# Optimization experiments

Measured on AMD Instinct MI355X. Metric: run time of the kernel, lower is better.

The kernel has to match this reference:

```python
import jax, jax.numpy as jnp
import numpy as np

N = 100000      # nodes
E = 3200000     # directed edges (avg degree 32)
F_IN, HID, CLS = 512, 256, 64


def setup_inputs() -> dict:
    key = jax.random.key(0)
    k = jax.random.split(key, 6)
    x = jax.random.normal(k[0], (N, F_IN), dtype=jnp.float32)
    edge_index = jax.random.randint(k[1], (2, E), 0, N, dtype=jnp.int32)
    W1 = jax.random.normal(k[2], (F_IN, HID), dtype=jnp.float32) / np.float32(np.sqrt(F_IN))
    b1 = jnp.zeros((HID,), dtype=jnp.float32)
    W2 = jax.random.normal(k[3], (HID, CLS), dtype=jnp.float32) / np.float32(np.sqrt(HID))
    b2 = jnp.zeros((CLS,), dtype=jnp.float32)
    return {"x": x, "edge_index": edge_index, "W1": W1, "b1": b1, "W2": W2, "b2": b2}


def gcn_layer(x, W, b, src, dst, n):
    """GCN layer: out = D^{-1/2} (A + I) D^{-1/2} (x W + b)."""
    h = x @ W + b                                   # [n, out]
    loop = jnp.arange(n, dtype=src.dtype)
    s = jnp.concatenate([src, loop])                # add self loops
    d = jnp.concatenate([dst, loop])
    deg = jax.ops.segment_sum(jnp.ones_like(d, dtype=h.dtype), d, num_segments=n)
    dinv = jax.lax.rsqrt(jnp.maximum(deg, 1.0))
    norm = dinv[s] * dinv[d]                        # [E+n]
    return jax.ops.segment_sum(h[s] * norm[:, None], d, num_segments=n)


def reference(x, edge_index, W1, b1, W2, b2):
    src, dst = edge_index[0], edge_index[1]
    n = x.shape[0]
    h = jax.nn.relu(gcn_layer(x, W1, b1, src, dst, n))
    # dropout is identity in eval mode
    h = gcn_layer(h, W2, b2, src, dst, n)
    return jax.nn.log_softmax(h, axis=1)
```

## Files before the change

kernel.cpp:

```cpp
#include <hip/hip_runtime.h>

#define FIN 512
#define HID 256
#define CLS 64
#define PAD 8
#define BKT_SLACK 4096

typedef short bf16x8 __attribute__((ext_vector_type(8)));
typedef float f32x4 __attribute__((ext_vector_type(4)));
typedef float f32x2 __attribute__((ext_vector_type(2)));

__device__ __forceinline__ float bf2f(unsigned short u) {
    union { unsigned int i; float f; } c; c.i = ((unsigned int)u) << 16; return c.f;
}
__device__ __forceinline__ unsigned short f2bf(float f) {
    union { float f; unsigned int u; } c; c.f = f;
    unsigned int u = c.u;
    return (unsigned short)((u + 0x7fffu + ((u >> 16) & 1u)) >> 16);
}
__device__ __forceinline__ unsigned char f2fp8(float v) {
    int r = __builtin_amdgcn_cvt_pk_fp8_f32(v, v, 0, false);
    return (unsigned char)(r & 0xFF);
}


__global__ __launch_bounds__(256) void k_hist(const int* __restrict__ dst,
                                              int* __restrict__ bktcnt, int E) {
    __shared__ int h[256];
    h[threadIdx.x] = 0;
    __syncthreads();
    for (int i = blockIdx.x * blockDim.x + threadIdx.x; i < E; i += gridDim.x * blockDim.x)
        atomicAdd(&h[dst[i] >> 9], 1);
    __syncthreads();
    if (h[threadIdx.x]) atomicAdd(&bktcnt[threadIdx.x], h[threadIdx.x]);
}

__global__ __launch_bounds__(256) void k_bktscan(const int* __restrict__ bktcnt,
                                                 int* __restrict__ bkt_base,
                                                 int* __restrict__ bkt_cursor,
                                                 int NB, int E) {
    __shared__ int sh[256];
    int t = threadIdx.x;
    int v = (t < NB) ? bktcnt[t] : 0;
    sh[t] = v;
    __syncthreads();
    for (int s = 1; s < 256; s <<= 1) {
        int u = (t >= s) ? sh[t - s] : 0;
        __syncthreads();
        sh[t] += u;
        __syncthreads();
    }
    int excl = sh[t] - v;
    if (t < NB) { bkt_base[t] = excl; bkt_cursor[t] = excl; }
    if (t == 0) bkt_base[NB] = E;
}

#define EPB 4096
__global__ __launch_bounds__(256) void k_binscatter(
        const int* __restrict__ src, const int* __restrict__ dst,
        int* __restrict__ bkt_cursor, uint2* __restrict__ ebuf, int E) {
    __shared__ int h[256];
    __shared__ int cb[256];
    int t = threadIdx.x;
    h[t] = 0;
    __syncthreads();
    int base = blockIdx.x * EPB;
    int es[16], ed[16], lp[16];
    #pragma unroll
    for (int it = 0; it < 16; ++it) {
        int i = base + it * 256 + t;
        if (i < E) {
            es[it] = src[i];
            ed[it] = dst[i];
            lp[it] = atomicAdd(&h[ed[it] >> 9], 1);
        } else {
            es[it] = -1; ed[it] = 0; lp[it] = 0;
        }
    }
    __syncthreads();
    int c = h[t];
    if (c) cb[t] = atomicAdd(&bkt_cursor[t], c);
    __syncthreads();
    #pragma unroll
    for (int it = 0; it < 16; ++it) {
        if (es[it] >= 0) {
            int b = ed[it] >> 9;
            ebuf[cb[b] + lp[it]] = make_uint2((unsigned)es[it], (unsigned)ed[it]);
        }
    }
}

__global__ __launch_bounds__(256) void k_csrbuild(
        const uint2* __restrict__ ebuf, const int* __restrict__ bkt_base,
        int* __restrict__ rs, int* __restrict__ cnte, float* __restrict__ dinv,
        int* __restrict__ csr, int Nn) {
    __shared__ int deg[512];
    __shared__ int cur[512];
    __shared__ int ts[256];
    int b = blockIdx.x, t = threadIdx.x;
    int e0 = bkt_base[b], e1 = bkt_base[b + 1];
    int pb = e0 + b * BKT_SLACK;
    int node0 = b << 9;
    deg[t] = 0; deg[t + 256] = 0;
    __syncthreads();
    for (int j = e0 + t; j < e1; j += 256)
        atomicAdd(&deg[(int)ebuf[j].y - node0], 1);
    __syncthreads();
    int n0 = node0 + 2 * t;
    int d0 = deg[2 * t], d1 = deg[2 * t + 1];
    int p0 = (n0 < Nn)     ? ((d0 + 1 + PAD - 1) & ~(PAD - 1)) : 0;
    int p1 = (n0 + 1 < Nn) ? ((d1 + 1 + PAD - 1) & ~(PAD - 1)) : 0;
    ts[t] = p0 + p1;
    __syncthreads();
    for (int s = 1; s < 256; s <<= 1) {
        int u = (t >= s) ? ts[t - s] : 0;
        __syncthreads();
        ts[t] += u;
        __syncthreads();
    }
    int excl = ts[t] - (p0 + p1);
    cur[2 * t] = excl;
    cur[2 * t + 1] = excl + p0;
    if (n0 < Nn)     { rs[n0]     = pb + excl;      cnte[n0]     = p0; dinv[n0]     = rsqrtf((float)(d0 + 1)); }
    if (n0 + 1 < Nn) { rs[n0 + 1] = pb + excl + p0; cnte[n0 + 1] = p1; dinv[n0 + 1] = rsqrtf((float)(d1 + 1)); }
    __syncthreads();
    for (int j = e0 + t; j < e1; j += 256) {
        uint2 e = ebuf[j];
        int p = atomicAdd(&cur[(int)e.y - node0], 1);
        csr[pb + p] = (int)e.x;
    }
    if (n0 < Nn) {
        csr[pb + excl + d0] = n0;
        for (int j = d0 + 1; j < p0; ++j) csr[pb + excl + j] = Nn;
    }
    if (n0 + 1 < Nn) {
        csr[pb + excl + p0 + d1] = n0 + 1;
        for (int j = d1 + 1; j < p1; ++j) csr[pb + excl + p0 + j] = Nn;
    }
}

__global__ void k_wpack(const float* __restrict__ W, unsigned short* __restrict__ Wp,
                        int K, int Ncols) {
    int i = blockIdx.x * blockDim.x + threadIdx.x;
    if (i < K * Ncols) {
        int k = i / Ncols, n = i - k * Ncols;
        Wp[((size_t)(k >> 3) * Ncols + n) * 8 + (k & 7)] = f2bf(W[i]);
    }
}

__global__ __launch_bounds__(512) void k_gemm1(
        const float* __restrict__ x, const unsigned short* __restrict__ W1p,
        const float* __restrict__ b1, const float* __restrict__ dinv,
        unsigned char* __restrict__ hs1, int Nn) {
    __shared__ unsigned short As[64][40];
    int tid = threadIdx.x;
    int w = tid >> 6, lane = tid & 63;
    int wr = w >> 2, wc = w & 3;
    int l15 = lane & 15, l4 = lane >> 4;
    int row0 = blockIdx.x * 64;

    f32x4 zero = {0.f, 0.f, 0.f, 0.f};
    f32x4 acc[2][4];
    #pragma unroll
    for (int m = 0; m < 2; ++m)
        #pragma unroll
        for (int n = 0; n < 4; ++n) acc[m][n] = zero;

    int sr = tid >> 3;
    int sc = tid & 7;
    bool srok = (row0 + sr) < Nn;
    const float* xrow = x + (size_t)(row0 + sr) * FIN + sc * 4;

    for (int kt = 0; kt < FIN; kt += 32) {
        float4 v = srok ? *(const float4*)(xrow + kt) : make_float4(0.f, 0.f, 0.f, 0.f);
        ushort4 o;
        o.x = f2bf(v.x); o.y = f2bf(v.y); o.z = f2bf(v.z); o.w = f2bf(v.w);
        *(ushort4*)&As[sr][sc * 4] = o;
        __syncthreads();

        bf16x8 bfr[4];
        size_t bbase = (size_t)((kt >> 3) + l4) * HID * 8;
        #pragma unroll
        for (int n = 0; n < 4; ++n) {
            int col = wc * 64 + n * 16 + l15;
            bfr[n] = *(const bf16x8*)&W1p[bbase + (size_t)col * 8];
        }
        bf16x8 afr[2];
        #pragma unroll
        for (int m = 0; m < 2; ++m) {
            int r = wr * 32 + m * 16 + l15;
            afr[m] = *(const bf16x8*)&As[r][l4 * 8];
        }
        #pragma unroll
        for (int m = 0; m < 2; ++m)
            #pragma unroll
            for (int n = 0; n < 4; ++n)
                acc[m][n] = __builtin_amdgcn_mfma_f32_16x16x32_bf16(
                    afr[m], bfr[n], acc[m][n], 0, 0, 0);
        __syncthreads();
    }

    float b1c[4];
    #pragma unroll
    for (int n = 0; n < 4; ++n) b1c[n] = b1[wc * 64 + n * 16 + l15];
    #pragma unroll
    for (int m = 0; m < 2; ++m) {
        #pragma unroll
        for (int r = 0; r < 4; ++r) {
            int row = row0 + wr * 32 + m * 16 + l4 * 4 + r;
            if (row < Nn) {
                float dv = dinv[row];
                #pragma unroll
                for (int n = 0; n < 4; ++n) {
                    int col = wc * 64 + n * 16 + l15;
                    hs1[(size_t)row * HID + col] = f2fp8((acc[m][n][r] + b1c[n]) * dv);
                }
            }
        }
    }
}

__global__ __launch_bounds__(256) void k_agg1(
        const unsigned char* __restrict__ hs1, const int* __restrict__ csr,
        const int* __restrict__ rs, const int* __restrict__ cnte,
        const float* __restrict__ dinv, unsigned short* __restrict__ h2in, int Nn) {
    int d = blockIdx.x * 4 + (threadIdx.x >> 6);
    if (d >= Nn) return;
    int lane = threadIdx.x & 63;
    int g = lane >> 4, c = lane & 15;
    size_t coff = (size_t)c * 16;
    float acc[16];
    #pragma unroll
    for (int j = 0; j < 16; ++j) acc[j] = 0.f;
    int base = rs[d], cnt = cnte[d];
    const int* cp = csr + base;
    int t = 0;
    for (; t + 16 <= cnt; t += 16) {
        int i0 = cp[t + g], i1 = cp[t + 4 + g], i2 = cp[t + 8 + g], i3 = cp[t + 12 + g];
        uint4 v0 = *(const uint4*)&hs1[(size_t)i0 * HID + coff];
        uint4 v1 = *(const uint4*)&hs1[(size_t)i1 * HID + coff];
        uint4 v2 = *(const uint4*)&hs1[(size_t)i2 * HID + coff];
        uint4 v3 = *(const uint4*)&hs1[(size_t)i3 * HID + coff];
        unsigned int w0[4] = {v0.x, v0.y, v0.z, v0.w};
        unsigned int w1[4] = {v1.x, v1.y, v1.z, v1.w};
        unsigned int w2[4] = {v2.x, v2.y, v2.z, v2.w};
        unsigned int w3[4] = {v3.x, v3.y, v3.z, v3.w};
        #pragma unroll
        for (int k = 0; k < 4; ++k) {
            f32x2 a0 = __builtin_amdgcn_cvt_pk_f32_fp8(w0[k], false);
            f32x2 b0 = __builtin_amdgcn_cvt_pk_f32_fp8(w0[k], true);
            f32x2 a1 = __builtin_amdgcn_cvt_pk_f32_fp8(w1[k], false);
            f32x2 b1v = __builtin_amdgcn_cvt_pk_f32_fp8(w1[k], true);
            f32x2 a2 = __builtin_amdgcn_cvt_pk_f32_fp8(w2[k], false);
            f32x2 b2v = __builtin_amdgcn_cvt_pk_f32_fp8(w2[k], true);
            f32x2 a3 = __builtin_amdgcn_cvt_pk_f32_fp8(w3[k], false);
            f32x2 b3 = __builtin_amdgcn_cvt_pk_f32_fp8(w3[k], true);
            acc[k*4+0] += (a0[0] + a1[0]) + (a2[0] + a3[0]);
            acc[k*4+1] += (a0[1] + a1[1]) + (a2[1] + a3[1]);
            acc[k*4+2] += (b0[0] + b1v[0]) + (b2v[0] + b3[0]);
            acc[k*4+3] += (b0[1] + b1v[1]) + (b2v[1] + b3[1]);
        }
    }
    if (t < cnt) {
        int i0 = cp[t + g], i1 = cp[t + 4 + g];
        uint4 v0 = *(const uint4*)&hs1[(size_t)i0 * HID + coff];
        uint4 v1 = *(const uint4*)&hs1[(size_t)i1 * HID + coff];
        unsigned int w0[4] = {v0.x, v0.y, v0.z, v0.w};
        unsigned int w1[4] = {v1.x, v1.y, v1.z, v1.w};
        #pragma unroll
        for (int k = 0; k < 4; ++k) {
            f32x2 a0 = __builtin_amdgcn_cvt_pk_f32_fp8(w0[k], false);
            f32x2 b0 = __builtin_amdgcn_cvt_pk_f32_fp8(w0[k], true);
            f32x2 a1 = __builtin_amdgcn_cvt_pk_f32_fp8(w1[k], false);
            f32x2 b1v = __builtin_amdgcn_cvt_pk_f32_fp8(w1[k], true);
            acc[k*4+0] += a0[0] + a1[0];
            acc[k*4+1] += a0[1] + a1[1];
            acc[k*4+2] += b0[0] + b1v[0];
            acc[k*4+3] += b0[1] + b1v[1];
        }
    }
    #pragma unroll
    for (int j = 0; j < 16; ++j) {
        acc[j] += __shfl_xor(acc[j], 16);
        acc[j] += __shfl_xor(acc[j], 32);
    }
    float dv = dinv[d];
    ushort4 o;
    o.x = f2bf(fmaxf(acc[g * 4 + 0] * dv, 0.f));
    o.y = f2bf(fmaxf(acc[g * 4 + 1] * dv, 0.f));
    o.z = f2bf(fmaxf(acc[g * 4 + 2] * dv, 0.f));
    o.w = f2bf(fmaxf(acc[g * 4 + 3] * dv, 0.f));
    *(ushort4*)&h2in[(size_t)d * HID + c * 16 + g * 4] = o;
}

__global__ __launch_bounds__(256) void k_gemm2(
        const unsigned short* __restrict__ h2in, const unsigned short* __restrict__ W2p,
        const float* __restrict__ b2, const float* __restrict__ dinv,
        unsigned short* __restrict__ hs2, int Nn) {
    int tid = threadIdx.x;
    int w = tid >> 6, lane = tid & 63;
    int l15 = lane & 15, l4 = lane >> 4;
    int r0 = blockIdx.x * 64 + w * 16;
    int arow = r0 + l15;
    bool aok = arow < Nn;
    const unsigned short* ap = h2in + (size_t)arow * HID + l4 * 8;

    f32x4 zero = {0.f, 0.f, 0.f, 0.f};
    bf16x8 zf = {0, 0, 0, 0, 0, 0, 0, 0};
    f32x4 acc[4];
    #pragma unroll
    for (int n = 0; n < 4; ++n) acc[n] = zero;

    #pragma unroll
    for (int kt = 0; kt < HID; kt += 32) {
        bf16x8 a = aok ? *(const bf16x8*)(ap + kt) : zf;
        size_t bbase = (size_t)((kt >> 3) + l4) * CLS * 8;
        #pragma unroll
        for (int n = 0; n < 4; ++n) {
            bf16x8 bb = *(const bf16x8*)&W2p[bbase + (size_t)(n * 16 + l15) * 8];
            acc[n] = __builtin_amdgcn_mfma_f32_16x16x32_bf16(a, bb, acc[n], 0, 0, 0);
        }
    }
    float b2c[4];
    #pragma unroll
    for (int n = 0; n < 4; ++n) b2c[n] = b2[n * 16 + l15];
    #pragma unroll
    for (int r = 0; r < 4; ++r) {
        int row = r0 + l4 * 4 + r;
        if (row < Nn) {
            float dv = dinv[row];
            #pragma unroll
            for (int n = 0; n < 4; ++n)
                hs2[(size_t)row * CLS + n * 16 + l15] = f2bf((acc[n][r] + b2c[n]) * dv);
        }
    }
}

__global__ __launch_bounds__(256) void k_agg2(
        const unsigned short* __restrict__ hs2, const int* __restrict__ csr,
        const int* __restrict__ rs, const int* __restrict__ cnte,
        const float* __restrict__ dinv, float* __restrict__ out, int Nn) {
    int d = blockIdx.x * 4 + (threadIdx.x >> 6);
    if (d >= Nn) return;
    int lane = threadIdx.x & 63;
    int q = lane >> 4, c4 = lane & 15;
    size_t loff = (size_t)c4 * 4;
    float a0 = 0.f, a1 = 0.f, a2 = 0.f, a3 = 0.f;
    int base = rs[d], cnt = cnte[d];
    const int* cp = csr + base;
    int t = 0;
    for (; t + 16 <= cnt; t += 16) {
        int s0 = cp[t + q], s1 = cp[t + q + 4], s2 = cp[t + q + 8], s3 = cp[t + q + 12];
        ushort4 v0 = *(const ushort4*)&hs2[(size_t)s0 * CLS + loff];
        ushort4 v1 = *(const ushort4*)&hs2[(size_t)s1 * CLS + loff];
        ushort4 v2 = *(const ushort4*)&hs2[(size_t)s2 * CLS + loff];
        ushort4 v3 = *(const ushort4*)&hs2[(size_t)s3 * CLS + loff];
        a0 += (bf2f(v0.x) + bf2f(v1.x)) + (bf2f(v2.x) + bf2f(v3.x));
        a1 += (bf2f(v0.y) + bf2f(v1.y)) + (bf2f(v2.y) + bf2f(v3.y));
        a2 += (bf2f(v0.z) + bf2f(v1.z)) + (bf2f(v2.z) + bf2f(v3.z));
        a3 += (bf2f(v0.w) + bf2f(v1.w)) + (bf2f(v2.w) + bf2f(v3.w));
    }
    if (t < cnt) {
        int s0 = cp[t + q], s1 = cp[t + q + 4];
        ushort4 v0 = *(const ushort4*)&hs2[(size_t)s0 * CLS + loff];
        ushort4 v1 = *(const ushort4*)&hs2[(size_t)s1 * CLS + loff];
        a0 += bf2f(v0.x) + bf2f(v1.x);
        a1 += bf2f(v0.y) + bf2f(v1.y);
        a2 += bf2f(v0.z) + bf2f(v1.z);
        a3 += bf2f(v0.w) + bf2f(v1.w);
    }
    a0 += __shfl_xor(a0, 16); a0 += __shfl_xor(a0, 32);
    a1 += __shfl_xor(a1, 16); a1 += __shfl_xor(a1, 32);
    a2 += __shfl_xor(a2, 16); a2 += __shfl_xor(a2, 32);
    a3 += __shfl_xor(a3, 16); a3 += __shfl_xor(a3, 32);
    float dv = dinv[d];
    float y0 = a0 * dv, y1 = a1 * dv, y2 = a2 * dv, y3 = a3 * dv;
    float m = fmaxf(fmaxf(y0, y1), fmaxf(y2, y3));
    #pragma unroll
    for (int o = 1; o <= 8; o <<= 1) m = fmaxf(m, __shfl_xor(m, o));
    float s = __expf(y0 - m) + __expf(y1 - m) + __expf(y2 - m) + __expf(y3 - m);
    #pragma unroll
    for (int o = 1; o <= 8; o <<= 1) s += __shfl_xor(s, o);
    if (q == 0) {
        float lg = __logf(s);
        float4 o4 = make_float4(y0 - m - lg, y1 - m - lg, y2 - m - lg, y3 - m - lg);
        *(float4*)&out[(size_t)d * CLS + c4 * 4] = o4;
    }
}

extern "C" void kernel_launch(void* const* d_in, const int* in_sizes, int n_in,
                              void* d_out, int out_size, void* d_ws, size_t ws_size,
                              hipStream_t stream) {
    const float* x  = (const float*)d_in[0];
    const int* ei   = (const int*)d_in[1];
    const float* W1 = (const float*)d_in[2];
    const float* b1 = (const float*)d_in[3];
    const float* W2 = (const float*)d_in[4];
    const float* b2 = (const float*)d_in[5];
    float* out = (float*)d_out;

    const int N = in_sizes[0] / FIN;
    const int E = in_sizes[1] / 2;
    const int NB = (N + 511) >> 9;
    const int* srcp = ei;
    const int* dstp = ei + E;

    char* w = (char*)d_ws;
    auto alloc = [&](size_t bytes) -> void* {
        void* p = (void*)w;
        w += (bytes + 255) / 256 * 256;
        return p;
    };
    int* rs        = (int*)alloc((size_t)(N + 1) * 4);
    int* cnte      = (int*)alloc((size_t)N * 4);
    float* dinv    = (float*)alloc((size_t)N * 4);
    int* csr       = (int*)alloc(((size_t)E + (size_t)N + (size_t)NB * BKT_SLACK + 8) * 4);
    int* bktcnt    = (int*)alloc((size_t)(NB + 1) * 4);
    int* bkt_base  = (int*)alloc((size_t)(NB + 1) * 4);
    int* bkt_cursor= (int*)alloc((size_t)(NB + 1) * 4);
    size_t hs1_bytes = (size_t)N * HID + HID;
    size_t ebuf_bytes = (size_t)E * 8;
    unsigned char* hs1 = (unsigned char*)alloc(hs1_bytes > ebuf_bytes ? hs1_bytes : ebuf_bytes + HID);
    unsigned short* h2in = (unsigned short*)alloc((size_t)N * HID * 2);
    unsigned short* hs2  = (unsigned short*)alloc((size_t)(N + 1) * CLS * 2);
    unsigned short* W1p  = (unsigned short*)alloc((size_t)FIN * HID * 2);
    unsigned short* W2p  = (unsigned short*)alloc((size_t)HID * CLS * 2);
    uint2* ebuf = (uint2*)hs1;

    hipMemsetAsync(bktcnt, 0, (size_t)(NB + 1) * 4, stream);

    k_hist<<<1024, 256, 0, stream>>>(dstp, bktcnt, E);
    k_bktscan<<<1, 256, 0, stream>>>(bktcnt, bkt_base, bkt_cursor, NB, E);
    k_binscatter<<<(E + EPB - 1) / EPB, 256, 0, stream>>>(srcp, dstp, bkt_cursor, ebuf, E);
    k_csrbuild<<<NB, 256, 0, stream>>>(ebuf, bkt_base, rs, cnte, dinv, csr, N);

    hipMemsetAsync(hs1 + (size_t)N * HID, 0, HID, stream);
    hipMemsetAsync(hs2 + (size_t)N * CLS, 0, CLS * 2, stream);

    k_wpack<<<(FIN * HID + 255) / 256, 256, 0, stream>>>(W1, W1p, FIN, HID);
    k_wpack<<<(HID * CLS + 255) / 256, 256, 0, stream>>>(W2, W2p, HID, CLS);

    k_gemm1<<<(N + 63) / 64, 512, 0, stream>>>(x, W1p, b1, dinv, hs1, N);
    k_agg1<<<(N + 3) / 4, 256, 0, stream>>>(hs1, csr, rs, cnte, dinv, h2in, N);
    k_gemm2<<<(N + 63) / 64, 256, 0, stream>>>(h2in, W2p, b2, dinv, hs2, N);
    k_agg2<<<(N + 3) / 4, 256, 0, stream>>>(hs2, csr, rs, cnte, dinv, out, N);
}
```

Baseline: 404.3 us.

## Split layer-1 features into column chunks for cache-resident aggregation passes

```diff
diff --git a/kernel.cpp b/kernel.cpp
--- a/kernel.cpp
+++ b/kernel.cpp
@@ -5,10 +5,12 @@
 #define CLS 64
 #define PAD 8
 #define BKT_SLACK 4096
+#define NCHUNK 8
 
 typedef short bf16x8 __attribute__((ext_vector_type(8)));
 typedef float f32x4 __attribute__((ext_vector_type(4)));
 typedef float f32x2 __attribute__((ext_vector_type(2)));
+typedef unsigned int u32x2 __attribute__((ext_vector_type(2)));
 
 __device__ __forceinline__ float bf2f(unsigned short u) {
     union { unsigned int i; float f; } c; c.i = ((unsigned int)u) << 16; return c.f;
@@ -58,7 +60,7 @@
 #define EPB 4096
 __global__ __launch_bounds__(256) void k_binscatter(
         const int* __restrict__ src, const int* __restrict__ dst,
-        int* __restrict__ bkt_cursor, uint2* __restrict__ ebuf, int E) {
+        int* __restrict__ bkt_cursor, unsigned* __restrict__ ebuf, int E) {
     __shared__ int h[256];
     __shared__ int cb[256];
     int t = threadIdx.x;
@@ -85,13 +87,13 @@
     for (int it = 0; it < 16; ++it) {
         if (es[it] >= 0) {
             int b = ed[it] >> 9;
-            ebuf[cb[b] + lp[it]] = make_uint2((unsigned)es[it], (unsigned)ed[it]);
+            ebuf[cb[b] + lp[it]] = (unsigned)es[it] | ((unsigned)(ed[it] & 511) << 23);
         }
     }
 }
 
 __global__ __launch_bounds__(256) void k_csrbuild(
-        const uint2* __restrict__ ebuf, const int* __restrict__ bkt_base,
+        const unsigned* __restrict__ ebuf, const int* __restrict__ bkt_base,
         int* __restrict__ rs, int* __restrict__ cnte, float* __restrict__ dinv,
         int* __restrict__ csr, int Nn) {
     __shared__ int deg[512];
@@ -104,7 +106,7 @@
     deg[t] = 0; deg[t + 256] = 0;
     __syncthreads();
     for (int j = e0 + t; j < e1; j += 256)
-        atomicAdd(&deg[(int)ebuf[j].y - node0], 1);
+        atomicAdd(&deg[ebuf[j] >> 23], 1);
     __syncthreads();
     int n0 = node0 + 2 * t;
     int d0 = deg[2 * t], d1 = deg[2 * t + 1];
@@ -125,9 +127,9 @@
     if (n0 + 1 < Nn) { rs[n0 + 1] = pb + excl + p0; cnte[n0 + 1] = p1; dinv[n0 + 1] = rsqrtf((float)(d1 + 1)); }
     __syncthreads();
     for (int j = e0 + t; j < e1; j += 256) {
-        uint2 e = ebuf[j];
-        int p = atomicAdd(&cur[(int)e.y - node0], 1);
-        csr[pb + p] = (int)e.x;
+        unsigned e = ebuf[j];
+        int p = atomicAdd(&cur[e >> 23], 1);
+        csr[pb + p] = (int)(e & 0x7FFFFFu);
     }
     if (n0 < Nn) {
         csr[pb + excl + d0] = n0;
@@ -158,6 +160,7 @@
     int wr = w >> 2, wc = w & 3;
     int l15 = lane & 15, l4 = lane >> 4;
     int row0 = blockIdx.x * 64;
+    size_t cstride = (size_t)(Nn + 1) * 32;
 
     f32x4 zero = {0.f, 0.f, 0.f, 0.f};
     f32x4 acc[2][4];
@@ -208,89 +211,69 @@
         #pragma unroll
         for (int r = 0; r < 4; ++r) {
             int row = row0 + wr * 32 + m * 16 + l4 * 4 + r;
-            if (row < Nn) {
-                float dv = dinv[row];
-                #pragma unroll
-                for (int n = 0; n < 4; ++n) {
-                    int col = wc * 64 + n * 16 + l15;
-                    hs1[(size_t)row * HID + col] = f2fp8((acc[m][n][r] + b1c[n]) * dv);
-                }
+            if (row > Nn) continue;
+            float dv = (row < Nn) ? dinv[row] : 0.f;
+            #pragma unroll
+            for (int n = 0; n < 4; ++n) {
+                int col = wc * 64 + n * 16 + l15;
+                unsigned char val = (row < Nn)
+                    ? f2fp8((acc[m][n][r] + b1c[n]) * dv) : (unsigned char)0;
+                hs1[(size_t)(col >> 5) * cstride + (size_t)row * 32 + (col & 31)] = val;
             }
         }
     }
 }
 
-__global__ __launch_bounds__(256) void k_agg1(
-        const unsigned char* __restrict__ hs1, const int* __restrict__ csr,
-        const int* __restrict__ rs, const int* __restrict__ cnte,
-        const float* __restrict__ dinv, unsigned short* __restrict__ h2in, int Nn) {
+__global__ __launch_bounds__(256) void k_agg1c(
+        const unsigned char* __restrict__ hs1c,
+        const int* __restrict__ csr, const int* __restrict__ rs,
+        const int* __restrict__ cnte, const float* __restrict__ dinv,
+        unsigned short* __restrict__ h2in, int Nn, int chunk) {
     int d = blockIdx.x * 4 + (threadIdx.x >> 6);
     if (d >= Nn) return;
     int lane = threadIdx.x & 63;
-    int g = lane >> 4, c = lane & 15;
-    size_t coff = (size_t)c * 16;
-    float acc[16];
-    #pragma unroll
-    for (int j = 0; j < 16; ++j) acc[j] = 0.f;
+    int g = lane >> 3;
+    int f = lane & 7;
     int base = rs[d], cnt = cnte[d];
     const int* cp = csr + base;
+    float a0 = 0.f, a1 = 0.f, a2 = 0.f, a3 = 0.f;
     int t = 0;
     for (; t + 16 <= cnt; t += 16) {
-        int i0 = cp[t + g], i1 = cp[t + 4 + g], i2 = cp[t + 8 + g], i3 = cp[t + 12 + g];
-        uint4 v0 = *(const uint4*)&hs1[(size_t)i0 * HID + coff];
-        uint4 v1 = *(const uint4*)&hs1[(size_t)i1 * HID + coff];
-        uint4 v2 = *(const uint4*)&hs1[(size_t)i2 * HID + coff];
-        uint4 v3 = *(const uint4*)&hs1[(size_t)i3 * HID + coff];
-        unsigned int w0[4] = {v0.x, v0.y, v0.z, v0.w};
-        unsigned int w1[4] = {v1.x, v1.y, v1.z, v1.w};
-        unsigned int w2[4] = {v2.x, v2.y, v2.z, v2.w};
-        unsigned int w3[4] = {v3.x, v3.y, v3.z, v3.w};
-        #pragma unroll
-        for (int k = 0; k < 4; ++k) {
-            f32x2 a0 = __builtin_amdgcn_cvt_pk_f32_fp8(w0[k], false);
-            f32x2 b0 = __builtin_amdgcn_cvt_pk_f32_fp8(w0[k], true);
-            f32x2 a1 = __builtin_amdgcn_cvt_pk_f32_fp8(w1[k], false);
-            f32x2 b1v = __builtin_amdgcn_cvt_pk_f32_fp8(w1[k], true);
-            f32x2 a2 = __builtin_amdgcn_cvt_pk_f32_fp8(w2[k], false);
-            f32x2 b2v = __builtin_amdgcn_cvt_pk_f32_fp8(w2[k], true);
-            f32x2 a3 = __builtin_amdgcn_cvt_pk_f32_fp8(w3[k], false);
-            f32x2 b3 = __builtin_amdgcn_cvt_pk_f32_fp8(w3[k], true);
-            acc[k*4+0] += (a0[0] + a1[0]) + (a2[0] + a3[0]);
-            acc[k*4+1] += (a0[1] + a1[1]) + (a2[1] + a3[1]);
-            acc[k*4+2] += (b0[0] + b1v[0]) + (b2v[0] + b3[0]);
-            acc[k*4+3] += (b0[1] + b1v[1]) + (b2v[1] + b3[1]);
-        }
+        int i0 = __builtin_nontemporal_load(&cp[t + g]);
+        int i1 = __builtin_nontemporal_load(&cp[t + 8 + g]);
+        unsigned v0 = *(const unsigned*)&hs1c[(size_t)i0 * 32 + f * 4];
+        unsigned v1 = *(const unsigned*)&hs1c[(size_t)i1 * 32 + f * 4];
+        f32x2 p00 = __builtin_amdgcn_cvt_pk_f32_fp8(v0, false);
+        f32x2 p01 = __builtin_amdgcn_cvt_pk_f32_fp8(v0, true);
+        f32x2 p10 = __builtin_amdgcn_cvt_pk_f32_fp8(v1, false);
+        f32x2 p11 = __builtin_amdgcn_cvt_pk_f32_fp8(v1, true);
+        a0 += p00[0] + p10[0];
+        a1 += p00[1] + p10[1];
+        a2 += p01[0] + p11[0];
+        a3 += p01[1] + p11[1];
     }
     if (t < cnt) {
-        int i0 = cp[t + g], i1 = cp[t + 4 + g];
-        uint4 v0 = *(const uint4*)&hs1[(size_t)i0 * HID + coff];
-        uint4 v1 = *(const uint4*)&hs1[(size_t)i1 * HID + coff];
-        unsigned int w0[4] = {v0.x, v0.y, v0.z, v0.w};
-        unsigned int w1[4] = {v1.x, v1.y, v1.z, v1.w};
-        #pragma unroll
-        for (int k = 0; k < 4; ++k) {
-            f32x2 a0 = __builtin_amdgcn_cvt_pk_f32_fp8(w0[k], false);
-            f32x2 b0 = __builtin_amdgcn_cvt_pk_f32_fp8(w0[k], true);
-            f32x2 a1 = __builtin_amdgcn_cvt_pk_f32_fp8(w1[k], false);
-            f32x2 b1v = __builtin_amdgcn_cvt_pk_f32_fp8(w1[k], true);
-            acc[k*4+0] += a0[0] + a1[0];
-            acc[k*4+1] += a0[1] + a1[1];
-            acc[k*4+2] += b0[0] + b1v[0];
-            acc[k*4+3] += b0[1] + b1v[1];
-        }
-    }
-    #pragma unroll
-    for (int j = 0; j < 16; ++j) {
-        acc[j] += __shfl_xor(acc[j], 16);
-        acc[j] += __shfl_xor(acc[j], 32);
-    }
-    float dv = dinv[d];
-    ushort4 o;
-    o.x = f2bf(fmaxf(acc[g * 4 + 0] * dv, 0.f));
-    o.y = f2bf(fmaxf(acc[g * 4 + 1] * dv, 0.f));
-    o.z = f2bf(fmaxf(acc[g * 4 + 2] * dv, 0.f));
-    o.w = f2bf(fmaxf(acc[g * 4 + 3] * dv, 0.f));
-    *(ushort4*)&h2in[(size_t)d * HID + c * 16 + g * 4] = o;
+        int i0 = __builtin_nontemporal_load(&cp[t + g]);
+        unsigned v0 = *(const unsigned*)&hs1c[(size_t)i0 * 32 + f * 4];
+        f32x2 p00 = __builtin_amdgcn_cvt_pk_f32_fp8(v0, false);
+        f32x2 p01 = __builtin_amdgcn_cvt_pk_f32_fp8(v0, true);
+        a0 += p00[0]; a1 += p00[1]; a2 += p01[0]; a3 += p01[1];
+    }
+    a0 += __shfl_xor(a0, 8); a0 += __shfl_xor(a0, 16); a0 += __shfl_xor(a0, 32);
+    a1 += __shfl_xor(a1, 8); a1 += __shfl_xor(a1, 16); a1 += __shfl_xor(a1, 32);
+    a2 += __shfl_xor(a2, 8); a2 += __shfl_xor(a2, 16); a2 += __shfl_xor(a2, 32);
+    a3 += __shfl_xor(a3, 8); a3 += __shfl_xor(a3, 16); a3 += __shfl_xor(a3, 32);
+    if (g == 0) {
+        float dv = dinv[d];
+        unsigned short o0 = f2bf(fmaxf(a0 * dv, 0.f));
+        unsigned short o1 = f2bf(fmaxf(a1 * dv, 0.f));
+        unsigned short o2 = f2bf(fmaxf(a2 * dv, 0.f));
+        unsigned short o3 = f2bf(fmaxf(a3 * dv, 0.f));
+        u32x2 u;
+        u[0] = (unsigned)o0 | ((unsigned)o1 << 16);
+        u[1] = (unsigned)o2 | ((unsigned)o3 << 16);
+        __builtin_nontemporal_store(u, (u32x2*)&h2in[(size_t)d * HID + chunk * 32 + f * 4]);
+    }
 }
 
 __global__ __launch_bounds__(256) void k_gemm2(
@@ -327,11 +310,13 @@
     #pragma unroll
     for (int r = 0; r < 4; ++r) {
         int row = r0 + l4 * 4 + r;
-        if (row < Nn) {
-            float dv = dinv[row];
-            #pragma unroll
-            for (int n = 0; n < 4; ++n)
-                hs2[(size_t)row * CLS + n * 16 + l15] = f2bf((acc[n][r] + b2c[n]) * dv);
+        if (row > Nn) continue;
+        float dv = (row < Nn) ? dinv[row] : 0.f;
+        #pragma unroll
+        for (int n = 0; n < 4; ++n) {
+            unsigned short val = (row < Nn)
+                ? f2bf((acc[n][r] + b2c[n]) * dv) : (unsigned short)0;
+            hs2[(size_t)row * CLS + n * 16 + l15] = val;
         }
     }
 }
@@ -350,7 +335,10 @@
     const int* cp = csr + base;
     int t = 0;
     for (; t + 16 <= cnt; t += 16) {
-        int s0 = cp[t + q], s1 = cp[t + q + 4], s2 = cp[t + q + 8], s3 = cp[t + q + 12];
+        int s0 = __builtin_nontemporal_load(&cp[t + q]);
+        int s1 = __builtin_nontemporal_load(&cp[t + q + 4]);
+        int s2 = __builtin_nontemporal_load(&cp[t + q + 8]);
+        int s3 = __builtin_nontemporal_load(&cp[t + q + 12]);
         ushort4 v0 = *(const ushort4*)&hs2[(size_t)s0 * CLS + loff];
         ushort4 v1 = *(const ushort4*)&hs2[(size_t)s1 * CLS + loff];
         ushort4 v2 = *(const ushort4*)&hs2[(size_t)s2 * CLS + loff];
@@ -361,7 +349,8 @@
         a3 += (bf2f(v0.w) + bf2f(v1.w)) + (bf2f(v2.w) + bf2f(v3.w));
     }
     if (t < cnt) {
-        int s0 = cp[t + q], s1 = cp[t + q + 4];
+        int s0 = __builtin_nontemporal_load(&cp[t + q]);
+        int s1 = __builtin_nontemporal_load(&cp[t + q + 4]);
         ushort4 v0 = *(const ushort4*)&hs2[(size_t)s0 * CLS + loff];
         ushort4 v1 = *(const ushort4*)&hs2[(size_t)s1 * CLS + loff];
         a0 += bf2f(v0.x) + bf2f(v1.x);
@@ -418,14 +407,15 @@
     int* bktcnt    = (int*)alloc((size_t)(NB + 1) * 4);
     int* bkt_base  = (int*)alloc((size_t)(NB + 1) * 4);
     int* bkt_cursor= (int*)alloc((size_t)(NB + 1) * 4);
-    size_t hs1_bytes = (size_t)N * HID + HID;
-    size_t ebuf_bytes = (size_t)E * 8;
-    unsigned char* hs1 = (unsigned char*)alloc(hs1_bytes > ebuf_bytes ? hs1_bytes : ebuf_bytes + HID);
+    size_t hs1_bytes = (size_t)NCHUNK * (N + 1) * 32;
+    size_t ebuf_bytes = (size_t)E * 4;
+    unsigned char* hs1 = (unsigned char*)alloc(hs1_bytes > ebuf_bytes ? hs1_bytes : ebuf_bytes);
     unsigned short* h2in = (unsigned short*)alloc((size_t)N * HID * 2);
     unsigned short* hs2  = (unsigned short*)alloc((size_t)(N + 1) * CLS * 2);
     unsigned short* W1p  = (unsigned short*)alloc((size_t)FIN * HID * 2);
     unsigned short* W2p  = (unsigned short*)alloc((size_t)HID * CLS * 2);
-    uint2* ebuf = (uint2*)hs1;
+    unsigned* ebuf = (unsigned*)hs1;
+    size_t cstride = (size_t)(N + 1) * 32;
 
     hipMemsetAsync(bktcnt, 0, (size_t)(NB + 1) * 4, stream);
 
@@ -434,14 +424,14 @@
     k_binscatter<<<(E + EPB - 1) / EPB, 256, 0, stream>>>(srcp, dstp, bkt_cursor, ebuf, E);
     k_csrbuild<<<NB, 256, 0, stream>>>(ebuf, bkt_base, rs, cnte, dinv, csr, N);
 
-    hipMemsetAsync(hs1 + (size_t)N * HID, 0, HID, stream);
-    hipMemsetAsync(hs2 + (size_t)N * CLS, 0, CLS * 2, stream);
-
     k_wpack<<<(FIN * HID + 255) / 256, 256, 0, stream>>>(W1, W1p, FIN, HID);
     k_wpack<<<(HID * CLS + 255) / 256, 256, 0, stream>>>(W2, W2p, HID, CLS);
 
-    k_gemm1<<<(N + 63) / 64, 512, 0, stream>>>(x, W1p, b1, dinv, hs1, N);
-    k_agg1<<<(N + 3) / 4, 256, 0, stream>>>(hs1, csr, rs, cnte, dinv, h2in, N);
-    k_gemm2<<<(N + 63) / 64, 256, 0, stream>>>(h2in, W2p, b2, dinv, hs2, N);
+    const int gemmGrid = (N + 64) / 64;
+    k_gemm1<<<gemmGrid, 512, 0, stream>>>(x, W1p, b1, dinv, hs1, N);
+    for (int c = 0; c < NCHUNK; ++c)
+        k_agg1c<<<(N + 3) / 4, 256, 0, stream>>>(hs1 + (size_t)c * cstride,
+                                                 csr, rs, cnte, dinv, h2in, N, c);
+    k_gemm2<<<gemmGrid, 256, 0, stream>>>(h2in, W2p, b2, dinv, hs2, N);
     k_agg2<<<(N + 3) / 4, 256, 0, stream>>>(hs2, csr, rs, cnte, dinv, out, N);
 }
```

After: 674.9 us. 66.9% more time.
